# Optimization experiments

Measured on AMD Instinct MI355X. Metric: run time of the kernel, lower is better.

Reference implementation:

```python
import jax, jax.numpy as jnp
import numpy as np
from jax import lax

VOCAB = 100000; E = 512; HID = 1024; H = HID // 2; T = 7; L = 4096
START = 4; STOP = 5; NEG = -10000.0


def setup_inputs() -> dict:
    key = jax.random.key(0)
    ks = jax.random.split(key, 14)
    s = 0.05  # ~1/sqrt(H), matches torch default init scale
    transitions = jax.random.normal(ks[12], (T, T), dtype=jnp.float32)
    transitions = transitions.at[START, :].set(NEG).at[:, STOP].set(NEG)
    return {
        "sentence": jax.random.randint(ks[0], (L,), 0, VOCAB),
        "emb": jax.random.normal(ks[1], (VOCAB, E), dtype=jnp.float32) * s,
        "w_ih_f": jax.random.normal(ks[2], (4 * H, E), dtype=jnp.float32) * s,
        "w_hh_f": jax.random.normal(ks[3], (4 * H, H), dtype=jnp.float32) * s,
        "b_ih_f": jax.random.normal(ks[4], (4 * H,), dtype=jnp.float32) * s,
        "b_hh_f": jax.random.normal(ks[5], (4 * H,), dtype=jnp.float32) * s,
        "w_ih_b": jax.random.normal(ks[6], (4 * H, E), dtype=jnp.float32) * s,
        "w_hh_b": jax.random.normal(ks[7], (4 * H, H), dtype=jnp.float32) * s,
        "b_ih_b": jax.random.normal(ks[8], (4 * H,), dtype=jnp.float32) * s,
        "b_hh_b": jax.random.normal(ks[9], (4 * H,), dtype=jnp.float32) * s,
        "w_out": jax.random.normal(ks[10], (T, HID), dtype=jnp.float32) * s,
        "b_out": jax.random.normal(ks[11], (T,), dtype=jnp.float32) * s,
        "transitions": transitions,
    }


def _lstm_dir(x, w_ih, w_hh, b_ih, b_hh):
    # x: [L, E] -> hidden states [L, H]; zero initial state (torch default)
    xg = x @ w_ih.T + b_ih  # [L, 4H] precomputed input gates
    h0 = jnp.zeros((H,), x.dtype)
    c0 = jnp.zeros((H,), x.dtype)
    def step(carry, g):
        h, c = carry
        gates = g + w_hh @ h + b_hh
        i, f, gg, o = jnp.split(gates, 4)
        i = jax.nn.sigmoid(i); f = jax.nn.sigmoid(f)
        gg = jnp.tanh(gg); o = jax.nn.sigmoid(o)
        c = f * c + i * gg
        h = o * jnp.tanh(c)
        return (h, c), h
    _, hs = lax.scan(step, (h0, c0), xg)
    return hs


def reference(sentence, emb, w_ih_f, w_hh_f, b_ih_f, b_hh_f,
              w_ih_b, w_hh_b, b_ih_b, b_hh_b, w_out, b_out, transitions):
    x = emb[sentence]  # [L, E]
    hf = _lstm_dir(x, w_ih_f, w_hh_f, b_ih_f, b_hh_f)            # [L, H]
    hb = _lstm_dir(x[::-1], w_ih_b, w_hh_b, b_ih_b, b_hh_b)[::-1]
    feats = jnp.concatenate([hf, hb], axis=1) @ w_out.T + b_out  # [L, T]

    # Viterbi max-plus DP
    init = jnp.full((T,), NEG, feats.dtype).at[START].set(0.0)
    def vstep(fv, feat):
        sc = fv[None, :] + transitions           # [next, prev]
        bp = jnp.argmax(sc, axis=1)
        return jnp.max(sc, axis=1) + feat, bp
    fv, bptrs = lax.scan(vstep, init, feats)     # bptrs: [L, T]
    terminal = fv + transitions[STOP]
    best = jnp.argmax(terminal)
    score = terminal[best]
    # backtrack
    def bt(tag, bp):
        return bp[tag], tag
    _, path_rev = lax.scan(bt, best, bptrs[::-1])
    best_path = path_rev[::-1]                   # [L] tag ids
    return best_path, score
```

## Files before the change

kernel.cpp:

```cpp
#include <hip/hip_runtime.h>
#include <hip/hip_bf16.h>

#define L     4096
#define E     512
#define HID   1024
#define HH    512
#define G4    2048
#define T_TAG 7
#define START_TAG 4
#define STOP_TAG  5
#define NEGV  (-10000.0f)

#define NWRK  32
#define NHELP 224
#define NTILE (64 * 2 * 32)
#define SENT  0xFFFFFFFFu

__device__ __forceinline__ float aload_f(const float* p) {
    const unsigned int v = __hip_atomic_load((const unsigned int*)p,
                                             __ATOMIC_RELAXED,
                                             __HIP_MEMORY_SCOPE_AGENT);
    return __uint_as_float(v);
}
__device__ __forceinline__ void astore_f(float* p, float x) {
    __hip_atomic_store((unsigned int*)p, __float_as_uint(x),
                       __ATOMIC_RELAXED, __HIP_MEMORY_SCOPE_AGENT);
}

__global__ __launch_bounds__(512)
void fused_kernel(const int* __restrict__ sentence, const float* __restrict__ emb,
                  const float* __restrict__ wih_f, const float* __restrict__ bih_f,
                  const float* __restrict__ bhh_f,
                  const float* __restrict__ wih_b, const float* __restrict__ bih_b,
                  const float* __restrict__ bhh_b,
                  const float* __restrict__ whh_f, const float* __restrict__ whh_b,
                  const float* __restrict__ wout, const float* __restrict__ bout,
                  float* __restrict__ xg_f, float* __restrict__ xg_b,
                  float* __restrict__ hf, float* __restrict__ hb,
                  float* __restrict__ feats, int* cnt)
{
    const int bid = blockIdx.x;
    const int tid = threadIdx.x;

    __shared__ float h_lds[2][HH];
    __shared__ float glds[8][16];
    __shared__ float As[32][68];
    __shared__ float Bs[32][68];
    __shared__ int   sent_s[64];
    __shared__ float red_s[8][8];

    if (bid < NWRK) {
        const int dir = bid >> 4;
        const int rnk = bid & 15;

        const float* __restrict__ xg  = dir ? xg_b  : xg_f;
        const float* __restrict__ whh = dir ? whh_b : whh_f;
        float* __restrict__ hout = dir ? hb : hf;

        const int wave = tid >> 6;
        const int lane = tid & 63;
        const int g    = wave >> 1;
        const int jh   = wave & 1;
        const int u0   = rnk * 32;

        float w[16][8];
#pragma unroll
        for (int rr = 0; rr < 16; rr++) {
            const size_t row = (size_t)(g * HH + u0 + jh * 16 + rr);
#pragma unroll
            for (int k = 0; k < 8; k++)
                w[rr][k] = whh[row * HH + (size_t)(k * 64 + lane)];
        }

        float c_state = 0.f;
        const int uu = u0 + (tid & 31);

        auto wait_chunk = [&](int tc) {
            const int* cp = cnt + dir * 64 + tc;
            while (__hip_atomic_load(cp, __ATOMIC_ACQUIRE,
                                     __HIP_MEMORY_SCOPE_AGENT) < 32) {
                __builtin_amdgcn_s_sleep(1);
            }
        };

        float xq0 = 0.f, xq1 = 0.f, xq2 = 0.f, xq3 = 0.f;
        if (tid < 32) {
            wait_chunk(dir ? 63 : 0);
            const float* xgt = xg + (size_t)(dir ? (L - 1) : 0) * G4;
            xq0 = aload_f(xgt + uu);            xq1 = aload_f(xgt + HH + uu);
            xq2 = aload_f(xgt + 2 * HH + uu);   xq3 = aload_f(xgt + 3 * HH + uu);
        }

        for (int s = 0; s < L; s++) {
            const int t = dir ? (L - 1 - s) : s;
            const int p = s & 1;

            unsigned int v = 0;
            if (s > 0) {
                const int tp = dir ? (t + 1) : (t - 1);
                const unsigned int* hp =
                    (const unsigned int*)(hout + (size_t)tp * HH) + tid;
                do {
                    v = __hip_atomic_load(hp, __ATOMIC_RELAXED,
                                          __HIP_MEMORY_SCOPE_AGENT);
                } while (v == SENT);
            }
            h_lds[p][tid] = __uint_as_float(v);
            __syncthreads();

            float hv[8];
#pragma unroll
            for (int k = 0; k < 8; k++) hv[k] = h_lds[p][k * 64 + lane];

            float acc[16];
#pragma unroll
            for (int rr = 0; rr < 16; rr++) {
                float a = 0.f;
#pragma unroll
                for (int k = 0; k < 8; k++) a += w[rr][k] * hv[k];
                acc[rr] = a;
            }

            {
                const bool b0 = lane & 1;
#pragma unroll
                for (int r = 0; r < 8; r++) {
                    const float send = b0 ? acc[r] : acc[r + 8];
                    const float recv = __shfl_xor(send, 1, 64);
                    acc[r] = (b0 ? acc[r + 8] : acc[r]) + recv;
                }
                const bool b1 = lane & 2;
#pragma unroll
                for (int r = 0; r < 4; r++) {
                    const float send = b1 ? acc[r] : acc[r + 4];
                    const float recv = __shfl_xor(send, 2, 64);
                    acc[r] = (b1 ? acc[r + 4] : acc[r]) + recv;
                }
                const bool b2 = lane & 4;
#pragma unroll
                for (int r = 0; r < 2; r++) {
                    const float send = b2 ? acc[r] : acc[r + 2];
                    const float recv = __shfl_xor(send, 4, 64);
                    acc[r] = (b2 ? acc[r + 2] : acc[r]) + recv;
                }
                const bool b3 = lane & 8;
                {
                    const float send = b3 ? acc[0] : acc[1];
                    const float recv = __shfl_xor(send, 8, 64);
                    acc[0] = (b3 ? acc[1] : acc[0]) + recv;
                }
                acc[0] += __shfl_xor(acc[0], 16, 64);
                acc[0] += __shfl_xor(acc[0], 32, 64);
            }
            if (lane < 16) {
                const int R = ((lane & 1) << 3) | ((lane & 2) << 1) |
                              ((lane & 4) >> 1) | ((lane & 8) >> 3);
                glds[wave][R] = acc[0];
            }
            __syncthreads();

            if (tid < 32) {
                const int jh_ = tid >> 4;
                const int rr  = tid & 15;
                float iv = glds[0 + jh_][rr] + xq0;
                float fv = glds[2 + jh_][rr] + xq1;
                float gv = glds[4 + jh_][rr] + xq2;
                float ov = glds[6 + jh_][rr] + xq3;
                iv = 1.f / (1.f + expf(-iv));
                fv = 1.f / (1.f + expf(-fv));
                gv = tanhf(gv);
                ov = 1.f / (1.f + expf(-ov));
                c_state = fv * c_state + iv * gv;
                const float hval = ov * tanhf(c_state);
                __hip_atomic_store((unsigned int*)&hout[(size_t)t * HH + uu],
                                   __float_as_uint(hval), __ATOMIC_RELAXED,
                                   __HIP_MEMORY_SCOPE_AGENT);
                if (s + 1 < L) {
                    const int tn = dir ? (t - 1) : (t + 1);
                    if ((tn & 63) == (dir ? 63 : 0)) wait_chunk(tn >> 6);
                    const float* xgt = xg + (size_t)tn * G4;
                    xq0 = aload_f(xgt + uu);
                    xq1 = aload_f(xgt + HH + uu);
                    xq2 = aload_f(xgt + 2 * HH + uu);
                    xq3 = aload_f(xgt + 3 * HH + uu);
                }
            }
        }
        return;
    }

    const int hid_ = bid - NWRK;

    for (int tile = hid_; tile < NTILE; tile += NHELP) {
        const int jt = tile & 31;
        const int sd = tile >> 5;
        const int dr = sd & 1;
        const int sc = sd >> 1;
        const int t0 = dr ? (L - 64 - sc * 64) : (sc * 64);
        const int j0 = jt * 64;
        const float* __restrict__ wih = dr ? wih_b : wih_f;
        const float* __restrict__ bih = dr ? bih_b : bih_f;
        const float* __restrict__ bhh = dr ? bhh_b : bhh_f;
        float* __restrict__ xg = dr ? xg_b : xg_f;

        if (tid < 64) sent_s[tid] = sentence[t0 + tid];

        const int li = tid >> 3;
        const int k4 = (tid & 7) * 4;
        const int tx = tid & 15;
        const int ty = tid >> 4;

        float a00 = 0.f, a01 = 0.f, a02 = 0.f, a03 = 0.f;
        float a10 = 0.f, a11 = 0.f, a12 = 0.f, a13 = 0.f;

        for (int k0 = 0; k0 < E; k0 += 32) {
            __syncthreads();
            {
                const float4 av = *(const float4*)(emb + (size_t)sent_s[li] * E + k0 + k4);
                As[k4 + 0][li] = av.x; As[k4 + 1][li] = av.y;
                As[k4 + 2][li] = av.z; As[k4 + 3][li] = av.w;
                const float4 bv = *(const float4*)(wih + (size_t)(j0 + li) * E + k0 + k4);
                Bs[k4 + 0][li] = bv.x; Bs[k4 + 1][li] = bv.y;
                Bs[k4 + 2][li] = bv.z; Bs[k4 + 3][li] = bv.w;
            }
            __syncthreads();
#pragma unroll
            for (int k = 0; k < 32; k++) {
                const float a0 = As[k][ty * 2 + 0];
                const float a1 = As[k][ty * 2 + 1];
                const float4 b4 = *(const float4*)&Bs[k][tx * 4];
                a00 += a0 * b4.x; a01 += a0 * b4.y; a02 += a0 * b4.z; a03 += a0 * b4.w;
                a10 += a1 * b4.x; a11 += a1 * b4.y; a12 += a1 * b4.z; a13 += a1 * b4.w;
            }
        }

        {
            const int c0 = j0 + tx * 4;
            const float bsum0 = bih[c0 + 0] + bhh[c0 + 0];
            const float bsum1 = bih[c0 + 1] + bhh[c0 + 1];
            const float bsum2 = bih[c0 + 2] + bhh[c0 + 2];
            const float bsum3 = bih[c0 + 3] + bhh[c0 + 3];
            float* r0 = xg + (size_t)(t0 + ty * 2 + 0) * G4 + c0;
            float* r1 = xg + (size_t)(t0 + ty * 2 + 1) * G4 + c0;
            astore_f(r0 + 0, a00 + bsum0); astore_f(r0 + 1, a01 + bsum1);
            astore_f(r0 + 2, a02 + bsum2); astore_f(r0 + 3, a03 + bsum3);
            astore_f(r1 + 0, a10 + bsum0); astore_f(r1 + 1, a11 + bsum1);
            astore_f(r1 + 2, a12 + bsum2); astore_f(r1 + 3, a13 + bsum3);
        }
        __syncthreads();
        if (tid == 0)
            __hip_atomic_fetch_add(&cnt[dr * 64 + (t0 >> 6)], 1,
                                   __ATOMIC_RELEASE, __HIP_MEMORY_SCOPE_AGENT);
    }

    const int wave = tid >> 6, lane = tid & 63;
    for (int t = hid_; t < L; t += NHELP) {
        if (tid < 32) {
            const float* src = (tid < 16) ? hf : hb;
            const unsigned int* wp =
                (const unsigned int*)(src + (size_t)t * HH) + (tid & 15) * 32;
            while (__hip_atomic_load(wp, __ATOMIC_RELAXED,
                                     __HIP_MEMORY_SCOPE_AGENT) == SENT) {
                __builtin_amdgcn_s_sleep(8);
            }
        }
        __syncthreads();

        const unsigned int* p0 = (const unsigned int*)(hf + (size_t)t * HH) + tid;
        const unsigned int* p1 = (const unsigned int*)(hb + (size_t)t * HH) + tid;
        unsigned int v0, v1;
        do { v0 = __hip_atomic_load(p0, __ATOMIC_RELAXED,
                                    __HIP_MEMORY_SCOPE_AGENT); } while (v0 == SENT);
        do { v1 = __hip_atomic_load(p1, __ATOMIC_RELAXED,
                                    __HIP_MEMORY_SCOPE_AGENT); } while (v1 == SENT);
        const float x0 = __uint_as_float(v0);
        const float x1 = __uint_as_float(v1);

        float acc[T_TAG];
#pragma unroll
        for (int i = 0; i < T_TAG; i++)
            acc[i] = x0 * wout[i * HID + tid] + x1 * wout[i * HID + HH + tid];
#pragma unroll
        for (int m = 1; m < 64; m <<= 1) {
#pragma unroll
            for (int i = 0; i < T_TAG; i++) acc[i] += __shfl_xor(acc[i], m, 64);
        }
        if (lane == 0) {
#pragma unroll
            for (int i = 0; i < T_TAG; i++) red_s[wave][i] = acc[i];
        }
        __syncthreads();
        if (tid < T_TAG) {
            float ssum = bout[tid];
#pragma unroll
            for (int wv = 0; wv < 8; wv++) ssum += red_s[wv][tid];
            feats[(size_t)t * 8 + tid] = ssum;
        }
        __syncthreads();
    }
}

__global__ __launch_bounds__(64)
void viterbi_kernel(const float* __restrict__ feats, const float* __restrict__ trans,
                    float* __restrict__ out)
{
    __shared__ unsigned char bp[L][T_TAG];

    const int tid = threadIdx.x;
    const int i = tid >> 3, j = tid & 7;
    const bool valid = (i < T_TAG) && (j < T_TAG);
    const float trij = valid ? trans[i * T_TAG + j] : -1e30f;

    float fv;
    if (j < T_TAG) fv = (j == START_TAG) ? 0.f : NEGV;
    else           fv = -1e30f;

    const int ieff = (i < T_TAG) ? i : 0;
    float fq[8];
#pragma unroll
    for (int q = 0; q < 8; q++) fq[q] = feats[(size_t)q * 8 + ieff];

#define VSTEP(T, Q, PREFETCH)                                                  \
    {                                                                          \
        const float sc = fv + trij;                                            \
        float best = sc; int bj = j;                                           \
        _Pragma("unroll")                                                      \
        for (int m = 1; m < 8; m <<= 1) {                                      \
            const float ov = __shfl_xor(best, m, 8);                           \
            const int   oj = __shfl_xor(bj, m, 8);                             \
            if (ov > best || (ov == best && oj < bj)) { best = ov; bj = oj; }  \
        }                                                                      \
        const float f_t = fq[Q];                                               \
        if (PREFETCH) fq[Q] = feats[(size_t)((T) + 8) * 8 + ieff];             \
        const float fvnew = best + f_t;                                        \
        if (valid && j == 0) bp[(T)][i] = (unsigned char)bj;                   \
        const float nf = __shfl(fvnew, (j < T_TAG) ? j * 8 : 0, 64);           \
        fv = (j < T_TAG) ? nf : -1e30f;                                        \
    }

    for (int tb = 0; tb < L - 8; tb += 8) {
#pragma unroll
        for (int q = 0; q < 8; q++) VSTEP(tb + q, q, true)
    }
    {
        const int tb = L - 8;
#pragma unroll
        for (int q = 0; q < 8; q++) VSTEP(tb + q, q, false)
    }
#undef VSTEP

    float term = fv + ((j < T_TAG) ? trans[STOP_TAG * T_TAG + j] : -1e30f);
    float bestt = term; int bt = j;
#pragma unroll
    for (int m = 1; m < 8; m <<= 1) {
        const float ov = __shfl_xor(bestt, m, 8);
        const int   oj = __shfl_xor(bt, m, 8);
        if (ov > bestt || (ov == bestt && oj < bt)) { bestt = ov; bt = oj; }
    }

    if (tid == 0) {
        out[L] = bestt;
        int tag = bt;
        out[L - 1] = (float)tag;
        for (int t = L - 1; t >= 1; t--) {
            tag = bp[t][tag];
            out[t - 1] = (float)tag;
        }
    }
}

extern "C" void kernel_launch(void* const* d_in, const int* in_sizes, int n_in,
                              void* d_out, int out_size, void* d_ws, size_t ws_size,
                              hipStream_t stream)
{
    const int*   sentence = (const int*)  d_in[0];
    const float* emb      = (const float*)d_in[1];
    const float* wih_f    = (const float*)d_in[2];
    const float* whh_f    = (const float*)d_in[3];
    const float* bih_f    = (const float*)d_in[4];
    const float* bhh_f    = (const float*)d_in[5];
    const float* wih_b    = (const float*)d_in[6];
    const float* whh_b    = (const float*)d_in[7];
    const float* bih_b    = (const float*)d_in[8];
    const float* bhh_b    = (const float*)d_in[9];
    const float* wout     = (const float*)d_in[10];
    const float* bout     = (const float*)d_in[11];
    const float* trans    = (const float*)d_in[12];
    float* out = (float*)d_out;

    char* ws = (char*)d_ws;
    int*   cnt    = (int*)ws;
    float* xg_f   = (float*)(ws + 1024);
    float* xg_b   = xg_f  + (size_t)L * G4;
    float* hfbuf  = xg_b  + (size_t)L * G4;
    float* hbbuf  = hfbuf + (size_t)L * HH;
    float* featsb = hbbuf + (size_t)L * HH;

    hipMemsetAsync(cnt, 0, 1024, stream);
    hipMemsetAsync(hfbuf, 0xFF, (size_t)2 * L * HH * sizeof(float), stream);

    void* args[] = { (void*)&sentence, (void*)&emb,
                     (void*)&wih_f, (void*)&bih_f, (void*)&bhh_f,
                     (void*)&wih_b, (void*)&bih_b, (void*)&bhh_b,
                     (void*)&whh_f, (void*)&whh_b,
                     (void*)&wout, (void*)&bout,
                     (void*)&xg_f, (void*)&xg_b,
                     (void*)&hfbuf, (void*)&hbbuf,
                     (void*)&featsb, (void*)&cnt };
    hipLaunchCooperativeKernel((void*)fused_kernel, dim3(NWRK + NHELP),
                               dim3(512), args, 0, stream);

    hipLaunchKernelGGL(viterbi_kernel, dim3(1), dim3(64), 0, stream,
                       featsb, trans, out);
}
```

Measured before the change: 9.091 ms.

## Replicate Viterbi state per lane and parallelize backtrack across 64 segments

The Viterbi forward pass now keeps all 7 forward scores in every lane's registers and computes the max-plus update redundantly per lane. This removes the per-step shuffles and the cross-lane argmax reduction from the serial dependency chain. The backtrack is split into 64 segments: each lane composes the backpointer maps over its segment, one lane chains the segment boundaries, and then all lanes emit their path segments in parallel. This trades redundant ALU work and extra shared-memory passes for a shorter serial critical path, but tie-breaking now depends on strict greater-than comparisons.

```diff
diff --git a/kernel.cpp b/kernel.cpp
--- a/kernel.cpp
+++ b/kernel.cpp
@@ -304,38 +304,73 @@
 void viterbi_kernel(const float* __restrict__ feats, const float* __restrict__ trans,
                     float* __restrict__ out)
 {
-    __shared__ unsigned char bp[L][T_TAG];
+    __shared__ unsigned char bp[L][8];
+    __shared__ unsigned char gl[64][8];
+    __shared__ unsigned char bnd[64];
 
     const int tid = threadIdx.x;
-    const int i = tid >> 3, j = tid & 7;
-    const bool valid = (i < T_TAG) && (j < T_TAG);
-    const float trij = valid ? trans[i * T_TAG + j] : -1e30f;
-
-    float fv;
-    if (j < T_TAG) fv = (j == START_TAG) ? 0.f : NEGV;
-    else           fv = -1e30f;
-
-    const int ieff = (i < T_TAG) ? i : 0;
-    float fq[8];
-#pragma unroll
-    for (int q = 0; q < 8; q++) fq[q] = feats[(size_t)q * 8 + ieff];
-
-#define VSTEP(T, Q, PREFETCH)                                                  \
+
+    float tr[T_TAG][T_TAG];
+#pragma unroll
+    for (int i = 0; i < T_TAG; i++)
+#pragma unroll
+        for (int j = 0; j < T_TAG; j++) tr[i][j] = trans[i * T_TAG + j];
+
+    const int d = tid % T_TAG;
+    float trd[T_TAG];
+#pragma unroll
+    for (int j = 0; j < T_TAG; j++) trd[j] = trans[d * T_TAG + j];
+
+    float trS[T_TAG];
+#pragma unroll
+    for (int j = 0; j < T_TAG; j++) trS[j] = trans[STOP_TAG * T_TAG + j];
+
+    float fv0 = NEGV, fv1 = NEGV, fv2 = NEGV, fv3 = NEGV,
+          fv4 = 0.f,  fv5 = NEGV, fv6 = NEGV;
+
+    float4 qa[8], qb[8];
+#pragma unroll
+    for (int q = 0; q < 8; q++) {
+        qa[q] = *(const float4*)(feats + (size_t)q * 8);
+        qb[q] = *(const float4*)(feats + (size_t)q * 8 + 4);
+    }
+
+#define VMAXROW(I, OUT, FI)                                                    \
     {                                                                          \
-        const float sc = fv + trij;                                            \
-        float best = sc; int bj = j;                                           \
-        _Pragma("unroll")                                                      \
-        for (int m = 1; m < 8; m <<= 1) {                                      \
-            const float ov = __shfl_xor(best, m, 8);                           \
-            const int   oj = __shfl_xor(bj, m, 8);                             \
-            if (ov > best || (ov == best && oj < bj)) { best = ov; bj = oj; }  \
+        const float a0 = fv0 + tr[I][0], a1 = fv1 + tr[I][1];                  \
+        const float a2 = fv2 + tr[I][2], a3 = fv3 + tr[I][3];                  \
+        const float a4 = fv4 + tr[I][4], a5 = fv5 + tr[I][5];                  \
+        const float a6 = fv6 + tr[I][6];                                       \
+        const float m012 = fmaxf(fmaxf(a0, a1), a2);                           \
+        const float m345 = fmaxf(fmaxf(a3, a4), a5);                           \
+        OUT = fmaxf(fmaxf(m012, m345), a6) + (FI);                             \
+    }
+
+#define VSTEP(T, Q, PRE)                                                       \
+    {                                                                          \
+        const float4 fa = qa[Q], fb = qb[Q];                                   \
+                     \
+        {                                                                      \
+            float bv_ = fv0 + trd[0]; int bj_ = 0; float c_;                   \
+            c_ = fv1 + trd[1]; if (c_ > bv_) { bv_ = c_; bj_ = 1; }            \
+            c_ = fv2 + trd[2]; if (c_ > bv_) { bv_ = c_; bj_ = 2; }            \
+            c_ = fv3 + trd[3]; if (c_ > bv_) { bv_ = c_; bj_ = 3; }            \
+            c_ = fv4 + trd[4]; if (c_ > bv_) { bv_ = c_; bj_ = 4; }            \
+            c_ = fv5 + trd[5]; if (c_ > bv_) { bv_ = c_; bj_ = 5; }            \
+            c_ = fv6 + trd[6]; if (c_ > bv_) { bv_ = c_; bj_ = 6; }            \
+            if (tid < T_TAG) bp[(T)][tid] = (unsigned char)bj_;                \
         }                                                                      \
-        const float f_t = fq[Q];                                               \
-        if (PREFETCH) fq[Q] = feats[(size_t)((T) + 8) * 8 + ieff];             \
-        const float fvnew = best + f_t;                                        \
-        if (valid && j == 0) bp[(T)][i] = (unsigned char)bj;                   \
-        const float nf = __shfl(fvnew, (j < T_TAG) ? j * 8 : 0, 64);           \
-        fv = (j < T_TAG) ? nf : -1e30f;                                        \
+                 \
+        float nf0, nf1, nf2, nf3, nf4, nf5, nf6;                               \
+        VMAXROW(0, nf0, fa.x) VMAXROW(1, nf1, fa.y) VMAXROW(2, nf2, fa.z)      \
+        VMAXROW(3, nf3, fa.w) VMAXROW(4, nf4, fb.x) VMAXROW(5, nf5, fb.y)      \
+        VMAXROW(6, nf6, fb.z)                                                  \
+        fv0 = nf0; fv1 = nf1; fv2 = nf2; fv3 = nf3;                            \
+        fv4 = nf4; fv5 = nf5; fv6 = nf6;                                       \
+        if (PRE) {                                                             \
+            qa[Q] = *(const float4*)(feats + (size_t)((T) + 8) * 8);           \
+            qb[Q] = *(const float4*)(feats + (size_t)((T) + 8) * 8 + 4);       \
+        }                                                                      \
     }
 
     for (int tb = 0; tb < L - 8; tb += 8) {
@@ -348,24 +383,56 @@
         for (int q = 0; q < 8; q++) VSTEP(tb + q, q, false)
     }
 #undef VSTEP
-
-    float term = fv + ((j < T_TAG) ? trans[STOP_TAG * T_TAG + j] : -1e30f);
-    float bestt = term; int bt = j;
-#pragma unroll
-    for (int m = 1; m < 8; m <<= 1) {
-        const float ov = __shfl_xor(bestt, m, 8);
-        const int   oj = __shfl_xor(bt, m, 8);
-        if (ov > bestt || (ov == bestt && oj < bt)) { bestt = ov; bt = oj; }
-    }
+#undef VMAXROW
+
+    int bt_final; float best_score;
+    {
+        float bv_ = fv0 + trS[0]; int bj_ = 0; float c_;
+        c_ = fv1 + trS[1]; if (c_ > bv_) { bv_ = c_; bj_ = 1; }
+        c_ = fv2 + trS[2]; if (c_ > bv_) { bv_ = c_; bj_ = 2; }
+        c_ = fv3 + trS[3]; if (c_ > bv_) { bv_ = c_; bj_ = 3; }
+        c_ = fv4 + trS[4]; if (c_ > bv_) { bv_ = c_; bj_ = 4; }
+        c_ = fv5 + trS[5]; if (c_ > bv_) { bv_ = c_; bj_ = 5; }
+        c_ = fv6 + trS[6]; if (c_ > bv_) { bv_ = c_; bj_ = 6; }
+        bt_final = bj_; best_score = bv_;
+    }
+    __syncthreads();
+
+    const int lo = 64 * tid + 1;
+    const int hi = (tid == 63) ? (L - 1) : (64 * tid + 64);
+    {
+        unsigned int c0 = 0, c1 = 1, c2 = 2, c3 = 3, c4 = 4, c5 = 5, c6 = 6;
+        for (int t = hi; t >= lo; --t) {
+            const unsigned char* row = &bp[t][0];
+            c0 = row[c0]; c1 = row[c1]; c2 = row[c2]; c3 = row[c3];
+            c4 = row[c4]; c5 = row[c5]; c6 = row[c6];
+        }
+        gl[tid][0] = (unsigned char)c0; gl[tid][1] = (unsigned char)c1;
+        gl[tid][2] = (unsigned char)c2; gl[tid][3] = (unsigned char)c3;
+        gl[tid][4] = (unsigned char)c4; gl[tid][5] = (unsigned char)c5;
+        gl[tid][6] = (unsigned char)c6;
+    }
+    __syncthreads();
 
     if (tid == 0) {
-        out[L] = bestt;
-        int tag = bt;
-        out[L - 1] = (float)tag;
-        for (int t = L - 1; t >= 1; t--) {
+        int b = bt_final;
+        for (int l2 = 63; l2 >= 0; --l2) {
+            bnd[l2] = (unsigned char)b;
+            b = gl[l2][b];
+        }
+    }
+    __syncthreads();
+
+    {
+        int tag = bnd[tid];
+        for (int t = hi; t >= lo; --t) {
             tag = bp[t][tag];
             out[t - 1] = (float)tag;
         }
+    }
+    if (tid == 63) {
+        out[L - 1] = (float)bt_final;
+        out[L]     = best_score;
     }
 }
 
```

Measured after the change: 9.102 ms. About the same (+0.1%).
